# Kernel tuning notes

Measured on AMD Instinct MI355X. Metric: run time of the kernel, lower is better.

Reference implementation:

```python
import jax, jax.numpy as jnp
import numpy as np

EPS = 1e-5


def conv1x1(x, w, b=None):
    # x: [B,C,H,W], w: [O,C] (1x1 conv kernel squeezed)
    y = jnp.einsum('bchw,oc->bohw', x, w)
    if b is not None:
        y = y + b[None, :, None, None]
    return y


def bn_inf(x, g, b, m, v):
    scale = g / jnp.sqrt(v + EPS)
    return (x - m[None, :, None, None]) * scale[None, :, None, None] + b[None, :, None, None]


def setup_inputs() -> dict:
    B, C, H, W = 2, 256, 80, 80
    Ck, Cv, Co = 64, 128, 256
    key = jax.random.key(0)
    ks = jax.random.split(key, 16)
    d = {}
    d['x'] = jax.random.normal(ks[0], (B, C, H, W), dtype=jnp.float32)
    d['y'] = jax.random.normal(ks[1], (B, C, H, W), dtype=jnp.float32)
    s = 1.0 / np.sqrt(C)
    d['fk_w'] = jax.random.normal(ks[2], (Ck, C), dtype=jnp.float32) * s
    d['fk_g'] = jnp.ones((Ck,), jnp.float32)
    d['fk_b'] = jnp.zeros((Ck,), jnp.float32)
    d['fk_m'] = jax.random.normal(ks[3], (Ck,), dtype=jnp.float32) * 0.1
    d['fk_v'] = jax.random.uniform(ks[4], (Ck,), minval=0.5, maxval=1.5, dtype=jnp.float32)
    d['fq_w'] = jax.random.normal(ks[5], (Ck, C), dtype=jnp.float32) * s
    d['fq_g'] = jnp.ones((Ck,), jnp.float32)
    d['fq_b'] = jnp.zeros((Ck,), jnp.float32)
    d['fq_m'] = jax.random.normal(ks[6], (Ck,), dtype=jnp.float32) * 0.1
    d['fq_v'] = jax.random.uniform(ks[7], (Ck,), minval=0.5, maxval=1.5, dtype=jnp.float32)
    d['fv_w'] = jax.random.normal(ks[8], (Cv, C), dtype=jnp.float32) * s
    d['fv_b'] = jnp.zeros((Cv,), jnp.float32)
    d['W_w'] = jax.random.normal(ks[9], (Co, Cv), dtype=jnp.float32) * (1.0 / np.sqrt(Cv))
    d['W_b'] = jnp.zeros((Co,), jnp.float32)
    d['gamma'] = jnp.array([0.5], jnp.float32)
    return d


def reference(x, y, fk_w, fk_g, fk_b, fk_m, fk_v, fq_w, fq_g, fq_b, fq_m, fq_v, fv_w, fv_b, W_w, W_b, gamma):
    B, C, H, W = x.shape
    Ck = fk_w.shape[0]
    Cv = fv_w.shape[0]
    N = H * W
    # key from x, query/value from y (1x1 conv + BN projections)
    k = bn_inf(conv1x1(x, fk_w), fk_g, fk_b, fk_m, fk_v).reshape(B, Ck, N)          # [B,Ck,N]
    q = bn_inf(conv1x1(y, fq_w), fq_g, fq_b, fq_m, fq_v).reshape(B, Ck, N)          # [B,Ck,N]
    v = conv1x1(y, fv_w, fv_b).reshape(B, Cv, N)                                     # [B,Cv,N]
    sim = jnp.einsum('bkn,bkm->bnm', q, k) * (Ck ** -0.5)                            # [B,N,N]
    sim = jax.nn.softmax(sim, axis=-1)
    ctx = jnp.einsum('bnm,bvm->bvn', sim, v).reshape(B, Cv, H, W)                    # [B,Cv,H,W]
    ctx = conv1x1(ctx, W_w, W_b)                                                     # [B,Co,H,W]
    return gamma[0] * ctx + x
```

## Files before the change

### kernel.cpp

```cpp
#include <hip/hip_runtime.h>
#include <math.h>

#define NB   2
#define CIN  256
#define NN   6400
#define CKd  64
#define CVd  128
#define COd  256

using bf16   = __bf16;
using bf16x4 = __attribute__((ext_vector_type(4))) bf16;
using bf16x8 = __attribute__((ext_vector_type(8))) bf16;
using f32x4  = __attribute__((ext_vector_type(4))) float;

__device__ __forceinline__ void lds_cp16(const void* g, void* l) {
    __builtin_amdgcn_global_load_lds((const __attribute__((address_space(1))) void*)g,
                                     (__attribute__((address_space(3))) void*)l, 16, 0, 0);
}

__launch_bounds__(256, 4)
__global__ void projkqv_kernel(const float* __restrict__ x, const float* __restrict__ y,
                               const float* __restrict__ fk_w, const float* __restrict__ fk_g,
                               const float* __restrict__ fk_b, const float* __restrict__ fk_m,
                               const float* __restrict__ fk_v,
                               const float* __restrict__ fq_w, const float* __restrict__ fq_g,
                               const float* __restrict__ fq_b, const float* __restrict__ fq_m,
                               const float* __restrict__ fq_v,
                               const float* __restrict__ fv_w, const float* __restrict__ fv_b,
                               bf16* __restrict__ kb, bf16* __restrict__ qb, bf16* __restrict__ vb)
{
    __shared__ __align__(16) bf16 sbuf[64 * 128];
    __shared__ __align__(16) bf16 wbuf[64 * 128];

    const int tid  = threadIdx.x;
    const int lane = tid & 63, wav = tid >> 6;
    const int l15  = lane & 15, quad = lane >> 4;
    const int b    = blockIdx.z, m = blockIdx.y;
    const int n0   = blockIdx.x * 64;
    const float QS = 0.18033688011112042f;

    const float* srcg = ((m == 0) ? x : y) + (size_t)b * CIN * NN;

    const int key = l15 & 7;
    f32x4 acc[4];
#pragma unroll
    for (int j = 0; j < 4; ++j) acc[j] = (f32x4){0.f, 0.f, 0.f, 0.f};

    for (int p = 0; p < 2; ++p) {
        if (p) __syncthreads();

        {
            const int r4  = lane >> 4;
            const int c16 = lane & 15;
#pragma unroll
            for (int i = 0; i < 4; ++i) {
                const int r  = wav * 16 + i * 4 + r4;
                const int cs = c16 ^ (r & 7);
                const float* ws = (m == 0) ? (fk_w + (size_t)r * CIN)
                                : (m == 1) ? (fq_w + (size_t)r * CIN)
                                : (fv_w + (size_t)((m - 2) * 64 + r) * CIN);
                const float4 w0 = *(const float4*)(ws + p * 128 + cs * 8);
                const float4 w1 = *(const float4*)(ws + p * 128 + cs * 8 + 4);
                float a = 1.0f;
                if (m == 0)      a = fk_g[r] * rsqrtf(fk_v[r] + 1e-5f);
                else if (m == 1) a = fq_g[r] * rsqrtf(fq_v[r] + 1e-5f) * QS;
                bf16x8 pk;
                pk[0] = (bf16)(w0.x * a); pk[1] = (bf16)(w0.y * a);
                pk[2] = (bf16)(w0.z * a); pk[3] = (bf16)(w0.w * a);
                pk[4] = (bf16)(w1.x * a); pk[5] = (bf16)(w1.y * a);
                pk[6] = (bf16)(w1.z * a); pk[7] = (bf16)(w1.w * a);
                *(bf16x8*)&wbuf[r * 128 + c16 * 8] = pk;
            }
        }
        {
            const int nl = (tid & 15) * 4;
            const int cq = tid >> 4;
            const int cb = p * 128 + cq * 8;
            float4 v[8];
#pragma unroll
            for (int e = 0; e < 8; ++e)
                v[e] = *(const float4*)(srcg + (size_t)(cb + e) * NN + n0 + nl);
#pragma unroll
            for (int i = 0; i < 4; ++i) {
                const int n = nl + i;
                bf16x8 pk;
#pragma unroll
                for (int e = 0; e < 8; ++e) pk[e] = (bf16)(&v[e].x)[i];
                *(bf16x8*)&sbuf[n * 128 + ((cq ^ (n & 7)) * 8)] = pk;
            }
        }
        __syncthreads();

        if (m < 2) {
            const int arow = wav * 16 + l15;
#pragma unroll
            for (int k4 = 0; k4 < 16; k4 += 4) {
                const bf16x8 af = *(const bf16x8*)&sbuf[arow * 128 + (((k4 + quad) ^ key) * 8)];
#pragma unroll
                for (int nt = 0; nt < 4; ++nt) {
                    const int brow = nt * 16 + l15;
                    const bf16x8 bfw = *(const bf16x8*)&wbuf[brow * 128 + (((k4 + quad) ^ key) * 8)];
                    acc[nt] = __builtin_amdgcn_mfma_f32_16x16x32_bf16(af, bfw, acc[nt], 0, 0, 0);
                }
            }
        } else {
            const int arow = wav * 16 + l15;
#pragma unroll
            for (int k4 = 0; k4 < 16; k4 += 4) {
                const bf16x8 af = *(const bf16x8*)&wbuf[arow * 128 + (((k4 + quad) ^ key) * 8)];
#pragma unroll
                for (int nt = 0; nt < 4; ++nt) {
                    const int brow = nt * 16 + l15;
                    const bf16x8 bfy = *(const bf16x8*)&sbuf[brow * 128 + (((k4 + quad) ^ key) * 8)];
                    acc[nt] = __builtin_amdgcn_mfma_f32_16x16x32_bf16(af, bfy, acc[nt], 0, 0, 0);
                }
            }
        }
    }

    if (m < 2) {
        bf16* dst = (m == 0) ? kb : qb;
        const int nb = n0 + wav * 16;
#pragma unroll
        for (int nt = 0; nt < 4; ++nt) {
            float bv;
            {
                const int c = nt * 16 + l15;
                if (m == 0) {
                    const float a = fk_g[c] * rsqrtf(fk_v[c] + 1e-5f);
                    bv = fk_b[c] - fk_m[c] * a;
                } else {
                    const float a = fq_g[c] * rsqrtf(fq_v[c] + 1e-5f);
                    bv = (fq_b[c] - fq_m[c] * a) * QS;
                }
            }
#pragma unroll
            for (int r = 0; r < 4; ++r) {
                const int n = nb + quad * 4 + r;
                dst[((size_t)b * NN + n) * CKd + nt * 16 + l15] = (bf16)(acc[nt][r] + bv);
            }
        }
    } else {
        const int cv0 = (m - 2) * 64 + wav * 16;
#pragma unroll
        for (int r = 0; r < 4; ++r) {
            const int cv = cv0 + quad * 4 + r;
            const float bv = fv_b[cv];
#pragma unroll
            for (int nt = 0; nt < 4; ++nt)
                vb[((size_t)b * CVd + cv) * NN + n0 + nt * 16 + l15] = (bf16)(acc[nt][r] + bv);
        }
    }
}

__launch_bounds__(256, 4)
__global__ void attn_kernel(const bf16* __restrict__ qb, const bf16* __restrict__ kb,
                            const bf16* __restrict__ vb,
                            bf16* __restrict__ pO, float* __restrict__ pl, int KS)
{
    __shared__ __align__(16) bf16 kbuf[2][64 * 64];
    __shared__ __align__(16) bf16 vbuf[128 * 64];
    __shared__ __align__(16) bf16 p_lds[4][16][64];

    const int lane = threadIdx.x & 63;
    const int wav  = threadIdx.x >> 6;
    const int l15  = lane & 15;
    const int quad = lane >> 4;
    const int r8   = lane >> 3;
    const int c_src = (lane & 7) ^ r8;
    const int sw   = l15 & 7;
    const int pkey = (l15 & 7) << 1;

    const int id    = blockIdx.x;
    const int ks    = id % KS;
    const int rst   = id / KS;
    const int b     = rst & 1;
    const int qtile = rst >> 1;
    const int q0    = qtile * 64 + wav * 16;

    const bf16* qrow = qb + (size_t)b * NN * CKd;
    const bf16* krow = kb + (size_t)b * NN * CKd;
    const bf16* vrow = vb + (size_t)b * CVd * NN;

    bf16x8 qf[2];
#pragma unroll
    for (int s = 0; s < 2; ++s)
        qf[s] = *(const bf16x8*)(qrow + (size_t)(q0 + l15) * CKd + s * 32 + quad * 8);

    const float ZC = -11.541560327111707f;
    const f32x4 zini = (f32x4){ZC, ZC, ZC, ZC};

    f32x4 acc[8];
#pragma unroll
    for (int cv = 0; cv < 8; ++cv) acc[cv] = (f32x4){0.f, 0.f, 0.f, 0.f};
    float psum = 0.f;

    const int t0 = (100 * ks) / KS;
    const int nt = (100 * (ks + 1)) / KS - t0;

    auto stageK = [&](int t, int bi) {
        const int key0 = t * 64;
        lds_cp16(krow + (size_t)(key0 + wav * 8 + r8) * CKd + c_src * 8,
                 &kbuf[bi][(wav * 8) * 64]);
        lds_cp16(krow + (size_t)(key0 + (wav + 4) * 8 + r8) * CKd + c_src * 8,
                 &kbuf[bi][((wav + 4) * 8) * 64]);
    };
    auto stageV = [&](int t) {
        const int key0 = t * 64;
#pragma unroll
        for (int g4 = 0; g4 < 4; ++g4) {
            const int g = wav * 4 + g4;
            lds_cp16(vrow + (size_t)(g * 8 + r8) * NN + key0 + c_src * 8,
                     &vbuf[(g * 8) * 64]);
        }
    };

    stageK(t0, 0);
    stageV(t0);
    __syncthreads();

    for (int t = 0; t < nt; ++t) {
        if (t + 1 < nt) stageK(t0 + t + 1, (t + 1) & 1);
        const bf16* kcur = &kbuf[t & 1][0];

        f32x4 s4[4];
#pragma unroll
        for (int kt = 0; kt < 4; ++kt) {
            const int rr = kt * 16 + l15;
            const bf16x8 kf0 = *(const bf16x8*)&kcur[rr * 64 + ((quad ^ sw) * 8)];
            const bf16x8 kf1 = *(const bf16x8*)&kcur[rr * 64 + (((4 + quad) ^ sw) * 8)];
            f32x4 z = zini;
            z = __builtin_amdgcn_mfma_f32_16x16x32_bf16(kf0, qf[0], z, 0, 0, 0);
            z = __builtin_amdgcn_mfma_f32_16x16x32_bf16(kf1, qf[1], z, 0, 0, 0);
            s4[kt] = z;
        }

#pragma unroll
        for (int kt = 0; kt < 4; ++kt) {
            bf16x4 pk;
#pragma unroll
            for (int r = 0; r < 4; ++r) {
                const float p = exp2f(s4[kt][r]);
                psum += p;
                pk[r] = (bf16)p;
            }
            *(bf16x4*)&p_lds[wav][l15][((kt * 4 + quad) ^ pkey) * 4] = pk;
        }

        if (t + 1 < nt) { asm volatile("s_waitcnt vmcnt(2)" ::: "memory"); }
        else            { asm volatile("s_waitcnt vmcnt(0)" ::: "memory"); }
        __builtin_amdgcn_s_barrier();

#pragma unroll
        for (int sp = 0; sp < 2; ++sp) {
            const bf16x8 pf = *(const bf16x8*)&p_lds[wav][l15][((sp * 8 + quad * 2) ^ pkey) * 4];
#pragma unroll
            for (int cvt = 0; cvt < 8; ++cvt) {
                const int rr = cvt * 16 + l15;
                const bf16x8 vf = *(const bf16x8*)&vbuf[rr * 64 + (((sp * 4 + quad) ^ sw) * 8)];
                acc[cvt] = __builtin_amdgcn_mfma_f32_16x16x32_bf16(vf, pf, acc[cvt], 0, 0, 0);
            }
        }

        __syncthreads();
        if (t + 1 < nt) stageV(t0 + t + 1);
    }

    psum += __shfl_xor(psum, 16);
    psum += __shfl_xor(psum, 32);
    bf16* tbuf = &vbuf[wav * 2048];
    const size_t pb = (size_t)ks * NB + b;
#pragma unroll
    for (int cvt = 0; cvt < 8; ++cvt) {
        bf16x4 pk;
#pragma unroll
        for (int r = 0; r < 4; ++r) pk[r] = (bf16)acc[cvt][r];
        const int u = (cvt * 4 + quad) ^ (l15 << 1);
        *(bf16x4*)&tbuf[l15 * 128 + u * 4] = pk;
    }
#pragma unroll
    for (int j = 0; j < 4; ++j) {
        const int row = j * 4 + (lane >> 4);
        const int g   = ((lane & 15) * 2) ^ ((row & 15) << 1);
        const bf16x8 vv = *(const bf16x8*)&tbuf[row * 128 + g * 4];
        *(bf16x8*)(pO + (pb * NN + q0 - wav * 16 + wav * 16) * CVd + j * 512 + lane * 8) = vv;
    }
    if (quad == 0) pl[pb * NN + q0 + l15] = psum;
}

__launch_bounds__(256, 4)
__global__ void outproj_kernel(const bf16* __restrict__ pO, const float* __restrict__ pl,
                               const float* __restrict__ W_w, const float* __restrict__ W_b,
                               const float* __restrict__ x, const float* __restrict__ gam,
                               float* __restrict__ out, int KS)
{
    __shared__ __align__(16) bf16 wbuf[128 * 128];
    __shared__ __align__(16) bf16 cbuf[32 * 128];

    const int tid  = threadIdx.x;
    const int lane = tid & 63, wav = tid >> 6;
    const int l15  = lane & 15, quad = lane >> 4;
    const int b    = blockIdx.y;
    const int n0   = blockIdx.x * 32;

    auto stage_w = [&](int p) {
        const int r4 = lane >> 4;
        const int c16 = lane & 15;
#pragma unroll
        for (int i = 0; i < 8; ++i) {
            const int r  = wav * 32 + i * 4 + r4;
            const int cs = c16 ^ (r & 7);
            const float* ws = W_w + (size_t)(p * 128 + r) * CVd + cs * 8;
            const float4 w0 = *(const float4*)(ws);
            const float4 w1 = *(const float4*)(ws + 4);
            bf16x8 pk;
            pk[0] = (bf16)w0.x; pk[1] = (bf16)w0.y; pk[2] = (bf16)w0.z; pk[3] = (bf16)w0.w;
            pk[4] = (bf16)w1.x; pk[5] = (bf16)w1.y; pk[6] = (bf16)w1.z; pk[7] = (bf16)w1.w;
            *(bf16x8*)&wbuf[r * 128 + c16 * 8] = pk;
        }
    };
    stage_w(0);

    const int tn = tid >> 3;
    const int tc = (tid & 7) * 16;
    const size_t kstr = (size_t)NB * NN * CVd;
    const bf16* src0 = pO + ((size_t)b * NN + n0 + tn) * CVd + tc;
    float vacc[16];
#pragma unroll
    for (int i = 0; i < 16; ++i) vacc[i] = 0.f;
    float L = 0.f;

    bf16x8 c0 = *(const bf16x8*)(src0);
    bf16x8 c1 = *(const bf16x8*)(src0 + 8);
    for (int ksi = 0; ksi < KS; ++ksi) {
        bf16x8 nx0 = c0, nx1 = c1;
        if (ksi + 1 < KS) {
            const bf16* s = src0 + (size_t)(ksi + 1) * kstr;
            nx0 = *(const bf16x8*)(s);
            nx1 = *(const bf16x8*)(s + 8);
        }
        L += pl[(size_t)(ksi * NB + b) * NN + n0 + tn];
#pragma unroll
        for (int e = 0; e < 8; ++e) vacc[e]     += (float)c0[e];
#pragma unroll
        for (int e = 0; e < 8; ++e) vacc[8 + e] += (float)c1[e];
        c0 = nx0; c1 = nx1;
    }
    {
        const float rL = 1.0f / L;
#pragma unroll
        for (int j = 0; j < 2; ++j) {
            bf16x8 o;
#pragma unroll
            for (int e = 0; e < 8; ++e) o[e] = (bf16)(vacc[j * 8 + e] * rL);
            const int c = (tid & 7) * 2 + j;
            *(bf16x8*)&cbuf[tn * 128 + ((c ^ (tn & 7)) * 8)] = o;
        }
    }
    __syncthreads();

    const float gm = gam[0];

    auto mfma_pass = [&](f32x4 (&acc)[2][2]) {
#pragma unroll
        for (int i = 0; i < 2; ++i)
#pragma unroll
            for (int j = 0; j < 2; ++j) acc[i][j] = (f32x4){0.f, 0.f, 0.f, 0.f};
#pragma unroll
        for (int kk = 0; kk < 4; ++kk) {
#pragma unroll
            for (int cot = 0; cot < 2; ++cot) {
                const int arow = wav * 32 + cot * 16 + l15;
                const bf16x8 af = *(const bf16x8*)&wbuf[arow * 128 + (((kk * 4 + quad) ^ (arow & 7)) * 8)];
#pragma unroll
                for (int nt = 0; nt < 2; ++nt) {
                    const int brow = nt * 16 + l15;
                    const bf16x8 bfc = *(const bf16x8*)&cbuf[brow * 128 + (((kk * 4 + quad) ^ (brow & 7)) * 8)];
                    acc[cot][nt] = __builtin_amdgcn_mfma_f32_16x16x32_bf16(af, bfc, acc[cot][nt], 0, 0, 0);
                }
            }
        }
    };
    auto store_pass = [&](const f32x4 (&acc)[2][2], int p) {
#pragma unroll
        for (int cot = 0; cot < 2; ++cot)
#pragma unroll
            for (int r = 0; r < 4; ++r) {
                const int co = p * 128 + wav * 32 + cot * 16 + quad * 4 + r;
                const float bv = W_b[co];
#pragma unroll
                for (int nt = 0; nt < 2; ++nt) {
                    const int n = n0 + nt * 16 + l15;
                    const size_t a = ((size_t)b * COd + co) * NN + n;
                    out[a] = gm * (acc[cot][nt][r] + bv) + x[a];
                }
            }
    };

    f32x4 acc0[2][2];
    mfma_pass(acc0);
    __syncthreads();
    stage_w(1);
    store_pass(acc0, 0);
    __syncthreads();
    f32x4 acc1[2][2];
    mfma_pass(acc1);
    store_pass(acc1, 1);
}

extern "C" void kernel_launch(void* const* d_in, const int* in_sizes, int n_in,
                              void* d_out, int out_size, void* d_ws, size_t ws_size,
                              hipStream_t stream)
{
    const float* x     = (const float*)d_in[0];
    const float* y     = (const float*)d_in[1];
    const float* fk_w  = (const float*)d_in[2];
    const float* fk_g  = (const float*)d_in[3];
    const float* fk_b  = (const float*)d_in[4];
    const float* fk_m  = (const float*)d_in[5];
    const float* fk_v  = (const float*)d_in[6];
    const float* fq_w  = (const float*)d_in[7];
    const float* fq_g  = (const float*)d_in[8];
    const float* fq_b  = (const float*)d_in[9];
    const float* fq_m  = (const float*)d_in[10];
    const float* fq_v  = (const float*)d_in[11];
    const float* fv_w  = (const float*)d_in[12];
    const float* fv_b  = (const float*)d_in[13];
    const float* W_w   = (const float*)d_in[14];
    const float* W_b   = (const float*)d_in[15];
    const float* gamma = (const float*)d_in[16];
    float* out = (float*)d_out;

    char* ws = (char*)d_ws;
    size_t off = 0;
    auto carve = [&](size_t bytes) -> char* {
        char* p = ws + off;
        off = (off + bytes + 255) & ~(size_t)255;
        return p;
    };

    bf16*  kb   = (bf16*)carve((size_t)NB * NN * CKd * 2);
    bf16*  qbuf = (bf16*)carve((size_t)NB * NN * CKd * 2);
    bf16*  vb   = (bf16*)carve((size_t)NB * CVd * NN * 2);

    const size_t region = ws_size - off;
    const size_t per_ks = (size_t)NB * NN * CVd * 2 + (size_t)NB * NN * 4 + 512;
    int KS = 1;
    {
        const int cand[4] = {5, 4, 2, 1};
        for (int i = 0; i < 4; ++i)
            if ((size_t)cand[i] * per_ks <= region) { KS = cand[i]; break; }
    }
    bf16*  pO = (bf16*)carve((size_t)KS * NB * NN * CVd * 2);
    float* pl = (float*)carve((size_t)KS * NB * NN * 4);

    const dim3 blk(256);
    projkqv_kernel<<<dim3(100, 4, NB), blk, 0, stream>>>(x, y,
                                                         fk_w, fk_g, fk_b, fk_m, fk_v,
                                                         fq_w, fq_g, fq_b, fq_m, fq_v,
                                                         fv_w, fv_b, kb, qbuf, vb);
    attn_kernel<<<dim3(100 * NB * KS), blk, 0, stream>>>(qbuf, kb, vb, pO, pl, KS);
    outproj_kernel<<<dim3(200, NB), blk, 0, stream>>>(pO, pl, W_w, W_b, x, gamma, out, KS);
}
```

Before: 167.9 us.

## Fuse projection, attention and output projection into one persistent kernel with grid barriers

Merges the three kernel launches into a single persistent kernel of 800 blocks that runs the projection, attention and output-projection phases, separated by software grid barriers built on atomic counters. The goal is to remove launch gaps and tail effects between kernels. The split-K count drops from 5 to 4 so that 800 blocks cover the 200*KS attention units exactly. Each output-projection block now handles one half of the output channels, where before one block did both halves. This relies on all 800 blocks being resident at once, else the barrier deadlocks. It also adds a memset launch to reset the barrier counters.

```diff
diff --git a/kernel.cpp b/kernel.cpp
--- a/kernel.cpp
+++ b/kernel.cpp
@@ -7,6 +7,7 @@
 #define CKd  64
 #define CVd  128
 #define COd  256
+#define GRID 800
 
 using bf16   = __bf16;
 using bf16x4 = __attribute__((ext_vector_type(4))) bf16;
@@ -18,350 +19,360 @@
                                      (__attribute__((address_space(3))) void*)l, 16, 0, 0);
 }
 
+__device__ __forceinline__ void grid_barrier(unsigned* bar, unsigned nblk) {
+    __syncthreads();
+    if (threadIdx.x == 0) {
+        __threadfence();
+        __hip_atomic_fetch_add(bar, 1u, __ATOMIC_ACQ_REL, __HIP_MEMORY_SCOPE_AGENT);
+        while (__hip_atomic_load(bar, __ATOMIC_ACQUIRE, __HIP_MEMORY_SCOPE_AGENT) < nblk)
+            __builtin_amdgcn_s_sleep(2);
+        __threadfence();
+    }
+    __syncthreads();
+}
+
 __launch_bounds__(256, 4)
-__global__ void projkqv_kernel(const float* __restrict__ x, const float* __restrict__ y,
-                               const float* __restrict__ fk_w, const float* __restrict__ fk_g,
-                               const float* __restrict__ fk_b, const float* __restrict__ fk_m,
-                               const float* __restrict__ fk_v,
-                               const float* __restrict__ fq_w, const float* __restrict__ fq_g,
-                               const float* __restrict__ fq_b, const float* __restrict__ fq_m,
-                               const float* __restrict__ fq_v,
-                               const float* __restrict__ fv_w, const float* __restrict__ fv_b,
-                               bf16* __restrict__ kb, bf16* __restrict__ qb, bf16* __restrict__ vb)
+__global__ void fused_kernel(
+    const float* __restrict__ x, const float* __restrict__ y,
+    const float* __restrict__ fk_w, const float* __restrict__ fk_g,
+    const float* __restrict__ fk_b, const float* __restrict__ fk_m,
+    const float* __restrict__ fk_v,
+    const float* __restrict__ fq_w, const float* __restrict__ fq_g,
+    const float* __restrict__ fq_b, const float* __restrict__ fq_m,
+    const float* __restrict__ fq_v,
+    const float* __restrict__ fv_w, const float* __restrict__ fv_b,
+    const float* __restrict__ W_w,  const float* __restrict__ W_b,
+    const float* __restrict__ gam,  float* __restrict__ out,
+    bf16* __restrict__ kb, bf16* __restrict__ qb, bf16* __restrict__ vb,
+    bf16* __restrict__ pO, float* __restrict__ pl,
+    unsigned* __restrict__ bars, int KS)
 {
-    __shared__ __align__(16) bf16 sbuf[64 * 128];
-    __shared__ __align__(16) bf16 wbuf[64 * 128];
+    __shared__ __align__(16) char smem[40960];
 
     const int tid  = threadIdx.x;
+    const int bid  = blockIdx.x;
     const int lane = tid & 63, wav = tid >> 6;
     const int l15  = lane & 15, quad = lane >> 4;
-    const int b    = blockIdx.z, m = blockIdx.y;
-    const int n0   = blockIdx.x * 64;
     const float QS = 0.18033688011112042f;
 
-    const float* srcg = ((m == 0) ? x : y) + (size_t)b * CIN * NN;
-
-    const int key = l15 & 7;
-    f32x4 acc[4];
-#pragma unroll
-    for (int j = 0; j < 4; ++j) acc[j] = (f32x4){0.f, 0.f, 0.f, 0.f};
-
-    for (int p = 0; p < 2; ++p) {
-        if (p) __syncthreads();
+    {
+        bf16* sbuf  = (bf16*)smem;
+        bf16* wbufP = (bf16*)(smem + 16384);
+
+        const int m  = (bid / 100) & 3;
+        const int b  = bid / 400;
+        const int n0 = (bid % 100) * 64;
+
+        const float* srcg = ((m == 0) ? x : y) + (size_t)b * CIN * NN;
+        const int key = l15 & 7;
+        f32x4 acc[4];
+#pragma unroll
+        for (int j = 0; j < 4; ++j) acc[j] = (f32x4){0.f, 0.f, 0.f, 0.f};
+
+        for (int p = 0; p < 2; ++p) {
+            if (p) __syncthreads();
+
+            {
+                const int r4  = lane >> 4;
+                const int c16 = lane & 15;
+#pragma unroll
+                for (int i = 0; i < 4; ++i) {
+                    const int r  = wav * 16 + i * 4 + r4;
+                    const int cs = c16 ^ (r & 7);
+                    const float* ws = (m == 0) ? (fk_w + (size_t)r * CIN)
+                                    : (m == 1) ? (fq_w + (size_t)r * CIN)
+                                    : (fv_w + (size_t)((m - 2) * 64 + r) * CIN);
+                    const float4 w0 = *(const float4*)(ws + p * 128 + cs * 8);
+                    const float4 w1 = *(const float4*)(ws + p * 128 + cs * 8 + 4);
+                    float a = 1.0f;
+                    if (m == 0)      a = fk_g[r] * rsqrtf(fk_v[r] + 1e-5f);
+                    else if (m == 1) a = fq_g[r] * rsqrtf(fq_v[r] + 1e-5f) * QS;
+                    bf16x8 pk;
+                    pk[0] = (bf16)(w0.x * a); pk[1] = (bf16)(w0.y * a);
+                    pk[2] = (bf16)(w0.z * a); pk[3] = (bf16)(w0.w * a);
+                    pk[4] = (bf16)(w1.x * a); pk[5] = (bf16)(w1.y * a);
+                    pk[6] = (bf16)(w1.z * a); pk[7] = (bf16)(w1.w * a);
+                    *(bf16x8*)&wbufP[r * 128 + c16 * 8] = pk;
+                }
+            }
+            {
+                const int nl = (tid & 15) * 4;
+                const int cq = tid >> 4;
+                const int cb = p * 128 + cq * 8;
+                float4 v[8];
+#pragma unroll
+                for (int e = 0; e < 8; ++e)
+                    v[e] = *(const float4*)(srcg + (size_t)(cb + e) * NN + n0 + nl);
+#pragma unroll
+                for (int i = 0; i < 4; ++i) {
+                    const int n = nl + i;
+                    bf16x8 pk;
+#pragma unroll
+                    for (int e = 0; e < 8; ++e) pk[e] = (bf16)(&v[e].x)[i];
+                    *(bf16x8*)&sbuf[n * 128 + ((cq ^ (n & 7)) * 8)] = pk;
+                }
+            }
+            __syncthreads();
+
+            if (m < 2) {
+                const int arow = wav * 16 + l15;
+#pragma unroll
+                for (int k4 = 0; k4 < 16; k4 += 4) {
+                    const bf16x8 af = *(const bf16x8*)&sbuf[arow * 128 + (((k4 + quad) ^ key) * 8)];
+#pragma unroll
+                    for (int nt = 0; nt < 4; ++nt) {
+                        const int brow = nt * 16 + l15;
+                        const bf16x8 bfw = *(const bf16x8*)&wbufP[brow * 128 + (((k4 + quad) ^ key) * 8)];
+                        acc[nt] = __builtin_amdgcn_mfma_f32_16x16x32_bf16(af, bfw, acc[nt], 0, 0, 0);
+                    }
+                }
+            } else {
+                const int arow = wav * 16 + l15;
+#pragma unroll
+                for (int k4 = 0; k4 < 16; k4 += 4) {
+                    const bf16x8 af = *(const bf16x8*)&wbufP[arow * 128 + (((k4 + quad) ^ key) * 8)];
+#pragma unroll
+                    for (int nt = 0; nt < 4; ++nt) {
+                        const int brow = nt * 16 + l15;
+                        const bf16x8 bfy = *(const bf16x8*)&sbuf[brow * 128 + (((k4 + quad) ^ key) * 8)];
+                        acc[nt] = __builtin_amdgcn_mfma_f32_16x16x32_bf16(af, bfy, acc[nt], 0, 0, 0);
+                    }
+                }
+            }
+        }
+
+        if (m < 2) {
+            bf16* dst = (m == 0) ? kb : qb;
+            const int nb = n0 + wav * 16;
+#pragma unroll
+            for (int nt = 0; nt < 4; ++nt) {
+                float bv;
+                {
+                    const int c = nt * 16 + l15;
+                    if (m == 0) {
+                        const float a = fk_g[c] * rsqrtf(fk_v[c] + 1e-5f);
+                        bv = fk_b[c] - fk_m[c] * a;
+                    } else {
+                        const float a = fq_g[c] * rsqrtf(fq_v[c] + 1e-5f);
+                        bv = (fq_b[c] - fq_m[c] * a) * QS;
+                    }
+                }
+#pragma unroll
+                for (int r = 0; r < 4; ++r) {
+                    const int n = nb + quad * 4 + r;
+                    dst[((size_t)b * NN + n) * CKd + nt * 16 + l15] = (bf16)(acc[nt][r] + bv);
+                }
+            }
+        } else {
+            const int cv0 = (m - 2) * 64 + wav * 16;
+#pragma unroll
+            for (int r = 0; r < 4; ++r) {
+                const int cv = cv0 + quad * 4 + r;
+                const float bv = fv_b[cv];
+#pragma unroll
+                for (int nt = 0; nt < 4; ++nt)
+                    vb[((size_t)b * CVd + cv) * NN + n0 + nt * 16 + l15] = (bf16)(acc[nt][r] + bv);
+            }
+        }
+    }
+
+    grid_barrier(&bars[0], GRID);
+
+    {
+        bf16* kbuf  = (bf16*)smem;
+        bf16* vbuf  = (bf16*)(smem + 16384);
+        bf16* p_lds = (bf16*)(smem + 32768);
+
+        const int r8    = lane >> 3;
+        const int c_src = (lane & 7) ^ r8;
+        const int sw    = l15 & 7;
+        const int pkey  = (l15 & 7) << 1;
+        const float ZC  = -11.541560327111707f;
+        const f32x4 zini = (f32x4){ZC, ZC, ZC, ZC};
+
+        for (int u = bid; u < 200 * KS; u += GRID) {
+            __syncthreads();
+            const int ks    = u % KS;
+            const int rst   = u / KS;
+            const int b     = rst & 1;
+            const int qtile = rst >> 1;
+            const int q0    = qtile * 64 + wav * 16;
+
+            const bf16* qrow = qb + (size_t)b * NN * CKd;
+            const bf16* krow = kb + (size_t)b * NN * CKd;
+            const bf16* vrow = vb + (size_t)b * CVd * NN;
+
+            bf16x8 qf[2];
+#pragma unroll
+            for (int s = 0; s < 2; ++s)
+                qf[s] = *(const bf16x8*)(qrow + (size_t)(q0 + l15) * CKd + s * 32 + quad * 8);
+
+            f32x4 acc[8];
+#pragma unroll
+            for (int cv = 0; cv < 8; ++cv) acc[cv] = (f32x4){0.f, 0.f, 0.f, 0.f};
+            float psum = 0.f;
+
+            const int t0 = (100 * ks) / KS;
+            const int nt = (100 * (ks + 1)) / KS - t0;
+
+            auto stageK = [&](int t, int bi) {
+                const int key0 = t * 64;
+                lds_cp16(krow + (size_t)(key0 + wav * 8 + r8) * CKd + c_src * 8,
+                         &kbuf[bi * 4096 + (wav * 8) * 64]);
+                lds_cp16(krow + (size_t)(key0 + (wav + 4) * 8 + r8) * CKd + c_src * 8,
+                         &kbuf[bi * 4096 + ((wav + 4) * 8) * 64]);
+            };
+            auto stageV = [&](int t) {
+                const int key0 = t * 64;
+#pragma unroll
+                for (int g4 = 0; g4 < 4; ++g4) {
+                    const int g = wav * 4 + g4;
+                    lds_cp16(vrow + (size_t)(g * 8 + r8) * NN + key0 + c_src * 8,
+                             &vbuf[(g * 8) * 64]);
+                }
+            };
+
+            stageK(t0, 0);
+            stageV(t0);
+            __syncthreads();
+
+            for (int t = 0; t < nt; ++t) {
+                if (t + 1 < nt) stageK(t0 + t + 1, (t + 1) & 1);
+                const bf16* kcur = &kbuf[(t & 1) * 4096];
+
+                f32x4 s4[4];
+#pragma unroll
+                for (int kt = 0; kt < 4; ++kt) {
+                    const int rr = kt * 16 + l15;
+                    const bf16x8 kf0 = *(const bf16x8*)&kcur[rr * 64 + ((quad ^ sw) * 8)];
+                    const bf16x8 kf1 = *(const bf16x8*)&kcur[rr * 64 + (((4 + quad) ^ sw) * 8)];
+                    f32x4 z = zini;
+                    z = __builtin_amdgcn_mfma_f32_16x16x32_bf16(kf0, qf[0], z, 0, 0, 0);
+                    z = __builtin_amdgcn_mfma_f32_16x16x32_bf16(kf1, qf[1], z, 0, 0, 0);
+                    s4[kt] = z;
+                }
+
+#pragma unroll
+                for (int kt = 0; kt < 4; ++kt) {
+                    bf16x4 pk;
+#pragma unroll
+                    for (int r = 0; r < 4; ++r) {
+                        const float p = exp2f(s4[kt][r]);
+                        psum += p;
+                        pk[r] = (bf16)p;
+                    }
+                    *(bf16x4*)&p_lds[(wav * 16 + l15) * 64 + ((kt * 4 + quad) ^ pkey) * 4] = pk;
+                }
+
+                if (t + 1 < nt) { asm volatile("s_waitcnt vmcnt(2)" ::: "memory"); }
+                else            { asm volatile("s_waitcnt vmcnt(0)" ::: "memory"); }
+                __builtin_amdgcn_s_barrier();
+
+#pragma unroll
+                for (int sp = 0; sp < 2; ++sp) {
+                    const bf16x8 pf = *(const bf16x8*)&p_lds[(wav * 16 + l15) * 64 + ((sp * 8 + quad * 2) ^ pkey) * 4];
+#pragma unroll
+                    for (int cvt = 0; cvt < 8; ++cvt) {
+                        const int rr = cvt * 16 + l15;
+                        const bf16x8 vf = *(const bf16x8*)&vbuf[rr * 64 + (((sp * 4 + quad) ^ sw) * 8)];
+                        acc[cvt] = __builtin_amdgcn_mfma_f32_16x16x32_bf16(vf, pf, acc[cvt], 0, 0, 0);
+                    }
+                }
+
+                __syncthreads();
+                if (t + 1 < nt) stageV(t0 + t + 1);
+            }
+
+            psum += __shfl_xor(psum, 16);
+            psum += __shfl_xor(psum, 32);
+            bf16* tbuf = &vbuf[wav * 2048];
+            const size_t pb = (size_t)ks * NB + b;
+#pragma unroll
+            for (int cvt = 0; cvt < 8; ++cvt) {
+                bf16x4 pk;
+#pragma unroll
+                for (int r = 0; r < 4; ++r) pk[r] = (bf16)acc[cvt][r];
+                const int uu = (cvt * 4 + quad) ^ (l15 << 1);
+                *(bf16x4*)&tbuf[l15 * 128 + uu * 4] = pk;
+            }
+#pragma unroll
+            for (int j = 0; j < 4; ++j) {
+                const int row = j * 4 + (lane >> 4);
+                const int g   = ((lane & 15) * 2) ^ ((row & 15) << 1);
+                const bf16x8 vv = *(const bf16x8*)&tbuf[row * 128 + g * 4];
+                *(bf16x8*)(pO + (pb * NN + q0) * CVd + j * 512 + lane * 8) = vv;
+            }
+            if (quad == 0) pl[pb * NN + q0 + l15] = psum;
+        }
+    }
+
+    grid_barrier(&bars[1], GRID);
+
+    {
+        bf16* wbufC = (bf16*)smem;
+        bf16* cbuf  = (bf16*)(smem + 32768);
+
+        const int b  = bid / 400;
+        const int n0 = ((bid >> 1) % 200) * 32;
+        const int p  = bid & 1;
 
         {
             const int r4  = lane >> 4;
             const int c16 = lane & 15;
 #pragma unroll
-            for (int i = 0; i < 4; ++i) {
-                const int r  = wav * 16 + i * 4 + r4;
+            for (int i = 0; i < 8; ++i) {
+                const int r  = wav * 32 + i * 4 + r4;
                 const int cs = c16 ^ (r & 7);
-                const float* ws = (m == 0) ? (fk_w + (size_t)r * CIN)
-                                : (m == 1) ? (fq_w + (size_t)r * CIN)
-                                : (fv_w + (size_t)((m - 2) * 64 + r) * CIN);
-                const float4 w0 = *(const float4*)(ws + p * 128 + cs * 8);
-                const float4 w1 = *(const float4*)(ws + p * 128 + cs * 8 + 4);
-                float a = 1.0f;
-                if (m == 0)      a = fk_g[r] * rsqrtf(fk_v[r] + 1e-5f);
-                else if (m == 1) a = fq_g[r] * rsqrtf(fq_v[r] + 1e-5f) * QS;
+                const float* ws = W_w + (size_t)(p * 128 + r) * CVd + cs * 8;
+                const float4 w0 = *(const float4*)(ws);
+                const float4 w1 = *(const float4*)(ws + 4);
                 bf16x8 pk;
-                pk[0] = (bf16)(w0.x * a); pk[1] = (bf16)(w0.y * a);
-                pk[2] = (bf16)(w0.z * a); pk[3] = (bf16)(w0.w * a);
-                pk[4] = (bf16)(w1.x * a); pk[5] = (bf16)(w1.y * a);
-                pk[6] = (bf16)(w1.z * a); pk[7] = (bf16)(w1.w * a);
-                *(bf16x8*)&wbuf[r * 128 + c16 * 8] = pk;
-            }
+                pk[0] = (bf16)w0.x; pk[1] = (bf16)w0.y; pk[2] = (bf16)w0.z; pk[3] = (bf16)w0.w;
+                pk[4] = (bf16)w1.x; pk[5] = (bf16)w1.y; pk[6] = (bf16)w1.z; pk[7] = (bf16)w1.w;
+                *(bf16x8*)&wbufC[r * 128 + c16 * 8] = pk;
+            }
+        }
+
+        const int tn = tid >> 3;
+        const int tc = (tid & 7) * 16;
+        const size_t kstr = (size_t)NB * NN * CVd;
+        const bf16* src0 = pO + ((size_t)b * NN + n0 + tn) * CVd + tc;
+        float vacc[16];
+#pragma unroll
+        for (int i = 0; i < 16; ++i) vacc[i] = 0.f;
+        float L = 0.f;
+
+        bf16x8 c0 = *(const bf16x8*)(src0);
+        bf16x8 c1 = *(const bf16x8*)(src0 + 8);
+        for (int ksi = 0; ksi < KS; ++ksi) {
+            bf16x8 nx0 = c0, nx1 = c1;
+            if (ksi + 1 < KS) {
+                const bf16* s = src0 + (size_t)(ksi + 1) * kstr;
+                nx0 = *(const bf16x8*)(s);
+                nx1 = *(const bf16x8*)(s + 8);
+            }
+            L += pl[(size_t)(ksi * NB + b) * NN + n0 + tn];
+#pragma unroll
+            for (int e = 0; e < 8; ++e) vacc[e]     += (float)c0[e];
+#pragma unroll
+            for (int e = 0; e < 8; ++e) vacc[8 + e] += (float)c1[e];
+            c0 = nx0; c1 = nx1;
         }
         {
-            const int nl = (tid & 15) * 4;
-            const int cq = tid >> 4;
-            const int cb = p * 128 + cq * 8;
-            float4 v[8];
-#pragma unroll
-            for (int e = 0; e < 8; ++e)
-                v[e] = *(const float4*)(srcg + (size_t)(cb + e) * NN + n0 + nl);
-#pragma unroll
-            for (int i = 0; i < 4; ++i) {
-                const int n = nl + i;
-                bf16x8 pk;
-#pragma unroll
-                for (int e = 0; e < 8; ++e) pk[e] = (bf16)(&v[e].x)[i];
-                *(bf16x8*)&sbuf[n * 128 + ((cq ^ (n & 7)) * 8)] = pk;
+            const float rL = 1.0f / L;
+#pragma unroll
+            for (int j = 0; j < 2; ++j) {
+                bf16x8 o;
+#pragma unroll
+                for (int e = 0; e < 8; ++e) o[e] = (bf16)(vacc[j * 8 + e] * rL);
+                const int c = (tid & 7) * 2 + j;
+                *(bf16x8*)&cbuf[tn * 128 + ((c ^ (tn & 7)) * 8)] = o;
             }
         }
         __syncthreads();
 
-        if (m < 2) {
-            const int arow = wav * 16 + l15;
-#pragma unroll
-            for (int k4 = 0; k4 < 16; k4 += 4) {
-                const bf16x8 af = *(const bf16x8*)&sbuf[arow * 128 + (((k4 + quad) ^ key) * 8)];
-#pragma unroll
-                for (int nt = 0; nt < 4; ++nt) {
-                    const int brow = nt * 16 + l15;
-                    const bf16x8 bfw = *(const bf16x8*)&wbuf[brow * 128 + (((k4 + quad) ^ key) * 8)];
-                    acc[nt] = __builtin_amdgcn_mfma_f32_16x16x32_bf16(af, bfw, acc[nt], 0, 0, 0);
-                }
-            }
-        } else {
-            const int arow = wav * 16 + l15;
-#pragma unroll
-            for (int k4 = 0; k4 < 16; k4 += 4) {
-                const bf16x8 af = *(const bf16x8*)&wbuf[arow * 128 + (((k4 + quad) ^ key) * 8)];
-#pragma unroll
-                for (int nt = 0; nt < 4; ++nt) {
-                    const int brow = nt * 16 + l15;
-                    const bf16x8 bfy = *(const bf16x8*)&sbuf[brow * 128 + (((k4 + quad) ^ key) * 8)];
-                    acc[nt] = __builtin_amdgcn_mfma_f32_16x16x32_bf16(af, bfy, acc[nt], 0, 0, 0);
-                }
-            }
-        }
-    }
-
-    if (m < 2) {
-        bf16* dst = (m == 0) ? kb : qb;
-        const int nb = n0 + wav * 16;
-#pragma unroll
-        for (int nt = 0; nt < 4; ++nt) {
-            float bv;
-            {
-                const int c = nt * 16 + l15;
-                if (m == 0) {
-                    const float a = fk_g[c] * rsqrtf(fk_v[c] + 1e-5f);
-                    bv = fk_b[c] - fk_m[c] * a;
-                } else {
-                    const float a = fq_g[c] * rsqrtf(fq_v[c] + 1e-5f);
-                    bv = (fq_b[c] - fq_m[c] * a) * QS;
-                }
-            }
-#pragma unroll
-            for (int r = 0; r < 4; ++r) {
-                const int n = nb + quad * 4 + r;
-                dst[((size_t)b * NN + n) * CKd + nt * 16 + l15] = (bf16)(acc[nt][r] + bv);
-            }
-        }
-    } else {
-        const int cv0 = (m - 2) * 64 + wav * 16;
-#pragma unroll
-        for (int r = 0; r < 4; ++r) {
-            const int cv = cv0 + quad * 4 + r;
-            const float bv = fv_b[cv];
-#pragma unroll
-            for (int nt = 0; nt < 4; ++nt)
-                vb[((size_t)b * CVd + cv) * NN + n0 + nt * 16 + l15] = (bf16)(acc[nt][r] + bv);
-        }
-    }
-}
-
-__launch_bounds__(256, 4)
-__global__ void attn_kernel(const bf16* __restrict__ qb, const bf16* __restrict__ kb,
-                            const bf16* __restrict__ vb,
-                            bf16* __restrict__ pO, float* __restrict__ pl, int KS)
-{
-    __shared__ __align__(16) bf16 kbuf[2][64 * 64];
-    __shared__ __align__(16) bf16 vbuf[128 * 64];
-    __shared__ __align__(16) bf16 p_lds[4][16][64];
-
-    const int lane = threadIdx.x & 63;
-    const int wav  = threadIdx.x >> 6;
-    const int l15  = lane & 15;
-    const int quad = lane >> 4;
-    const int r8   = lane >> 3;
-    const int c_src = (lane & 7) ^ r8;
-    const int sw   = l15 & 7;
-    const int pkey = (l15 & 7) << 1;
-
-    const int id    = blockIdx.x;
-    const int ks    = id % KS;
-    const int rst   = id / KS;
-    const int b     = rst & 1;
-    const int qtile = rst >> 1;
-    const int q0    = qtile * 64 + wav * 16;
-
-    const bf16* qrow = qb + (size_t)b * NN * CKd;
-    const bf16* krow = kb + (size_t)b * NN * CKd;
-    const bf16* vrow = vb + (size_t)b * CVd * NN;
-
-    bf16x8 qf[2];
-#pragma unroll
-    for (int s = 0; s < 2; ++s)
-        qf[s] = *(const bf16x8*)(qrow + (size_t)(q0 + l15) * CKd + s * 32 + quad * 8);
-
-    const float ZC = -11.541560327111707f;
-    const f32x4 zini = (f32x4){ZC, ZC, ZC, ZC};
-
-    f32x4 acc[8];
-#pragma unroll
-    for (int cv = 0; cv < 8; ++cv) acc[cv] = (f32x4){0.f, 0.f, 0.f, 0.f};
-    float psum = 0.f;
-
-    const int t0 = (100 * ks) / KS;
-    const int nt = (100 * (ks + 1)) / KS - t0;
-
-    auto stageK = [&](int t, int bi) {
-        const int key0 = t * 64;
-        lds_cp16(krow + (size_t)(key0 + wav * 8 + r8) * CKd + c_src * 8,
-                 &kbuf[bi][(wav * 8) * 64]);
-        lds_cp16(krow + (size_t)(key0 + (wav + 4) * 8 + r8) * CKd + c_src * 8,
-                 &kbuf[bi][((wav + 4) * 8) * 64]);
-    };
-    auto stageV = [&](int t) {
-        const int key0 = t * 64;
-#pragma unroll
-        for (int g4 = 0; g4 < 4; ++g4) {
-            const int g = wav * 4 + g4;
-            lds_cp16(vrow + (size_t)(g * 8 + r8) * NN + key0 + c_src * 8,
-                     &vbuf[(g * 8) * 64]);
-        }
-    };
-
-    stageK(t0, 0);
-    stageV(t0);
-    __syncthreads();
-
-    for (int t = 0; t < nt; ++t) {
-        if (t + 1 < nt) stageK(t0 + t + 1, (t + 1) & 1);
-        const bf16* kcur = &kbuf[t & 1][0];
-
-        f32x4 s4[4];
-#pragma unroll
-        for (int kt = 0; kt < 4; ++kt) {
-            const int rr = kt * 16 + l15;
-            const bf16x8 kf0 = *(const bf16x8*)&kcur[rr * 64 + ((quad ^ sw) * 8)];
-            const bf16x8 kf1 = *(const bf16x8*)&kcur[rr * 64 + (((4 + quad) ^ sw) * 8)];
-            f32x4 z = zini;
-            z = __builtin_amdgcn_mfma_f32_16x16x32_bf16(kf0, qf[0], z, 0, 0, 0);
-            z = __builtin_amdgcn_mfma_f32_16x16x32_bf16(kf1, qf[1], z, 0, 0, 0);
-            s4[kt] = z;
-        }
-
-#pragma unroll
-        for (int kt = 0; kt < 4; ++kt) {
-            bf16x4 pk;
-#pragma unroll
-            for (int r = 0; r < 4; ++r) {
-                const float p = exp2f(s4[kt][r]);
-                psum += p;
-                pk[r] = (bf16)p;
-            }
-            *(bf16x4*)&p_lds[wav][l15][((kt * 4 + quad) ^ pkey) * 4] = pk;
-        }
-
-        if (t + 1 < nt) { asm volatile("s_waitcnt vmcnt(2)" ::: "memory"); }
-        else            { asm volatile("s_waitcnt vmcnt(0)" ::: "memory"); }
-        __builtin_amdgcn_s_barrier();
-
-#pragma unroll
-        for (int sp = 0; sp < 2; ++sp) {
-            const bf16x8 pf = *(const bf16x8*)&p_lds[wav][l15][((sp * 8 + quad * 2) ^ pkey) * 4];
-#pragma unroll
-            for (int cvt = 0; cvt < 8; ++cvt) {
-                const int rr = cvt * 16 + l15;
-                const bf16x8 vf = *(const bf16x8*)&vbuf[rr * 64 + (((sp * 4 + quad) ^ sw) * 8)];
-                acc[cvt] = __builtin_amdgcn_mfma_f32_16x16x32_bf16(vf, pf, acc[cvt], 0, 0, 0);
-            }
-        }
-
-        __syncthreads();
-        if (t + 1 < nt) stageV(t0 + t + 1);
-    }
-
-    psum += __shfl_xor(psum, 16);
-    psum += __shfl_xor(psum, 32);
-    bf16* tbuf = &vbuf[wav * 2048];
-    const size_t pb = (size_t)ks * NB + b;
-#pragma unroll
-    for (int cvt = 0; cvt < 8; ++cvt) {
-        bf16x4 pk;
-#pragma unroll
-        for (int r = 0; r < 4; ++r) pk[r] = (bf16)acc[cvt][r];
-        const int u = (cvt * 4 + quad) ^ (l15 << 1);
-        *(bf16x4*)&tbuf[l15 * 128 + u * 4] = pk;
-    }
-#pragma unroll
-    for (int j = 0; j < 4; ++j) {
-        const int row = j * 4 + (lane >> 4);
-        const int g   = ((lane & 15) * 2) ^ ((row & 15) << 1);
-        const bf16x8 vv = *(const bf16x8*)&tbuf[row * 128 + g * 4];
-        *(bf16x8*)(pO + (pb * NN + q0 - wav * 16 + wav * 16) * CVd + j * 512 + lane * 8) = vv;
-    }
-    if (quad == 0) pl[pb * NN + q0 + l15] = psum;
-}
-
-__launch_bounds__(256, 4)
-__global__ void outproj_kernel(const bf16* __restrict__ pO, const float* __restrict__ pl,
-                               const float* __restrict__ W_w, const float* __restrict__ W_b,
-                               const float* __restrict__ x, const float* __restrict__ gam,
-                               float* __restrict__ out, int KS)
-{
-    __shared__ __align__(16) bf16 wbuf[128 * 128];
-    __shared__ __align__(16) bf16 cbuf[32 * 128];
-
-    const int tid  = threadIdx.x;
-    const int lane = tid & 63, wav = tid >> 6;
-    const int l15  = lane & 15, quad = lane >> 4;
-    const int b    = blockIdx.y;
-    const int n0   = blockIdx.x * 32;
-
-    auto stage_w = [&](int p) {
-        const int r4 = lane >> 4;
-        const int c16 = lane & 15;
-#pragma unroll
-        for (int i = 0; i < 8; ++i) {
-            const int r  = wav * 32 + i * 4 + r4;
-            const int cs = c16 ^ (r & 7);
-            const float* ws = W_w + (size_t)(p * 128 + r) * CVd + cs * 8;
-            const float4 w0 = *(const float4*)(ws);
-            const float4 w1 = *(const float4*)(ws + 4);
-            bf16x8 pk;
-            pk[0] = (bf16)w0.x; pk[1] = (bf16)w0.y; pk[2] = (bf16)w0.z; pk[3] = (bf16)w0.w;
-            pk[4] = (bf16)w1.x; pk[5] = (bf16)w1.y; pk[6] = (bf16)w1.z; pk[7] = (bf16)w1.w;
-            *(bf16x8*)&wbuf[r * 128 + c16 * 8] = pk;
-        }
-    };
-    stage_w(0);
-
-    const int tn = tid >> 3;
-    const int tc = (tid & 7) * 16;
-    const size_t kstr = (size_t)NB * NN * CVd;
-    const bf16* src0 = pO + ((size_t)b * NN + n0 + tn) * CVd + tc;
-    float vacc[16];
-#pragma unroll
-    for (int i = 0; i < 16; ++i) vacc[i] = 0.f;
-    float L = 0.f;
-
-    bf16x8 c0 = *(const bf16x8*)(src0);
-    bf16x8 c1 = *(const bf16x8*)(src0 + 8);
-    for (int ksi = 0; ksi < KS; ++ksi) {
-        bf16x8 nx0 = c0, nx1 = c1;
-        if (ksi + 1 < KS) {
-            const bf16* s = src0 + (size_t)(ksi + 1) * kstr;
-            nx0 = *(const bf16x8*)(s);
-            nx1 = *(const bf16x8*)(s + 8);
-        }
-        L += pl[(size_t)(ksi * NB + b) * NN + n0 + tn];
-#pragma unroll
-        for (int e = 0; e < 8; ++e) vacc[e]     += (float)c0[e];
-#pragma unroll
-        for (int e = 0; e < 8; ++e) vacc[8 + e] += (float)c1[e];
-        c0 = nx0; c1 = nx1;
-    }
-    {
-        const float rL = 1.0f / L;
-#pragma unroll
-        for (int j = 0; j < 2; ++j) {
-            bf16x8 o;
-#pragma unroll
-            for (int e = 0; e < 8; ++e) o[e] = (bf16)(vacc[j * 8 + e] * rL);
-            const int c = (tid & 7) * 2 + j;
-            *(bf16x8*)&cbuf[tn * 128 + ((c ^ (tn & 7)) * 8)] = o;
-        }
-    }
-    __syncthreads();
-
-    const float gm = gam[0];
-
-    auto mfma_pass = [&](f32x4 (&acc)[2][2]) {
+        const float gm = gam[0];
+        f32x4 acc[2][2];
 #pragma unroll
         for (int i = 0; i < 2; ++i)
 #pragma unroll
@@ -371,7 +382,7 @@
 #pragma unroll
             for (int cot = 0; cot < 2; ++cot) {
                 const int arow = wav * 32 + cot * 16 + l15;
-                const bf16x8 af = *(const bf16x8*)&wbuf[arow * 128 + (((kk * 4 + quad) ^ (arow & 7)) * 8)];
+                const bf16x8 af = *(const bf16x8*)&wbufC[arow * 128 + (((kk * 4 + quad) ^ (arow & 7)) * 8)];
 #pragma unroll
                 for (int nt = 0; nt < 2; ++nt) {
                     const int brow = nt * 16 + l15;
@@ -380,10 +391,8 @@
                 }
             }
         }
-    };
-    auto store_pass = [&](const f32x4 (&acc)[2][2], int p) {
-#pragma unroll
-        for (int cot = 0; cot < 2; ++cot)
+#pragma unroll
+        for (int cot = 0; cot < 2; ++cot) {
 #pragma unroll
             for (int r = 0; r < 4; ++r) {
                 const int co = p * 128 + wav * 32 + cot * 16 + quad * 4 + r;
@@ -395,17 +404,8 @@
                     out[a] = gm * (acc[cot][nt][r] + bv) + x[a];
                 }
             }
-    };
-
-    f32x4 acc0[2][2];
-    mfma_pass(acc0);
-    __syncthreads();
-    stage_w(1);
-    store_pass(acc0, 0);
-    __syncthreads();
-    f32x4 acc1[2][2];
-    mfma_pass(acc1);
-    store_pass(acc1, 1);
+        }
+    }
 }
 
 extern "C" void kernel_launch(void* const* d_in, const int* in_sizes, int n_in,
@@ -439,6 +439,7 @@
         return p;
     };
 
+    unsigned* bars = (unsigned*)carve(256);
     bf16*  kb   = (bf16*)carve((size_t)NB * NN * CKd * 2);
     bf16*  qbuf = (bf16*)carve((size_t)NB * NN * CKd * 2);
     bf16*  vb   = (bf16*)carve((size_t)NB * CVd * NN * 2);
@@ -447,18 +448,19 @@
     const size_t per_ks = (size_t)NB * NN * CVd * 2 + (size_t)NB * NN * 4 + 512;
     int KS = 1;
     {
-        const int cand[4] = {5, 4, 2, 1};
-        for (int i = 0; i < 4; ++i)
+        const int cand[3] = {4, 2, 1};
+        for (int i = 0; i < 3; ++i)
             if ((size_t)cand[i] * per_ks <= region) { KS = cand[i]; break; }
     }
     bf16*  pO = (bf16*)carve((size_t)KS * NB * NN * CVd * 2);
     float* pl = (float*)carve((size_t)KS * NB * NN * 4);
 
-    const dim3 blk(256);
-    projkqv_kernel<<<dim3(100, 4, NB), blk, 0, stream>>>(x, y,
-                                                         fk_w, fk_g, fk_b, fk_m, fk_v,
-                                                         fq_w, fq_g, fq_b, fq_m, fq_v,
-                                                         fv_w, fv_b, kb, qbuf, vb);
-    attn_kernel<<<dim3(100 * NB * KS), blk, 0, stream>>>(qbuf, kb, vb, pO, pl, KS);
-    outproj_kernel<<<dim3(200, NB), blk, 0, stream>>>(pO, pl, W_w, W_b, x, gamma, out, KS);
+    hipMemsetAsync(bars, 0, 256, stream);
+
+    fused_kernel<<<dim3(GRID), dim3(256), 0, stream>>>(
+        x, y,
+        fk_w, fk_g, fk_b, fk_m, fk_v,
+        fq_w, fq_g, fq_b, fq_m, fq_v,
+        fv_w, fv_b, W_w, W_b, gamma, out,
+        kb, qbuf, vb, pO, pl, bars, KS);
 }
```

Result: slower. 530.3 us (+216.0%).
